# Optimization experiments

Measured on AMD Instinct MI355X. Metric: run time of the kernel, lower is better.

## Reference

```python
import jax, jax.numpy as jnp
import numpy as np

H = 128; D = 16; L = 4
NP_ = 50000; NL_ = 10000; EPP = 500000; ELP = 100000; EPL = 100000


def _rbf(d):
    # GaussianSmearing(start=0, stop=8, num_gaussians=16)
    off = jnp.linspace(0.0, 8.0, D)
    coeff = -0.5 / ((8.0 / (D - 1)) ** 2)
    x = d[:, None] - off[None, :]
    return jnp.exp(coeff * x * x)


def _layer_norm(x, w, b, eps=1e-5):
    mu = jnp.mean(x, axis=-1, keepdims=True)
    var = jnp.var(x, axis=-1, keepdims=True)
    return (x - mu) * jax.lax.rsqrt(var + eps) * w + b


def _block(x_src, x_dst, src, dst, ea, Wf_, bf_, Ws_, bs_, bnw, bnb, lnw, lnb):
    # CGConv message: z = [x_i(dst), x_j(src), edge_attr]
    z = jnp.concatenate([x_dst[dst], x_src[src], ea], axis=-1)  # [E, 2H+D]
    m = jax.nn.sigmoid(z @ Wf_ + bf_) * jax.nn.softplus(z @ Ws_ + bs_)
    agg = jax.ops.segment_sum(m, dst, num_segments=x_dst.shape[0])
    # BatchNorm1d in eval mode with running_mean=0, running_var=1
    agg = agg * (bnw / jnp.sqrt(1.0 + 1e-5)) + bnb
    out = agg + x_dst            # CGConv internal residual
    out = _layer_norm(out, lnw, lnb)
    out = jax.nn.relu(out)
    return out + x_dst           # ResidualCGConvBlock residual (dropout=identity in eval)


def setup_inputs() -> dict:
    key = jax.random.key(0)
    ks = jax.random.split(key, 16)
    s = lambda n: 1.0 / np.sqrt(n)
    inp = {
        'x_protein': jax.random.normal(ks[0], (NP_, 6), jnp.float32),
        'x_ligand': jax.random.normal(ks[1], (NL_, 6), jnp.float32),
        'ei_pp': jnp.stack([jax.random.randint(ks[2], (EPP,), 0, NP_),
                            jax.random.randint(ks[3], (EPP,), 0, NP_)]).astype(jnp.int32),
        'ea_pp': jax.random.uniform(ks[4], (EPP,), jnp.float32, 0.0, 8.0),
        'ei_lp': jnp.stack([jax.random.randint(ks[5], (ELP,), 0, NL_),
                            jax.random.randint(ks[6], (ELP,), 0, NP_)]).astype(jnp.int32),
        'ea_lp': jax.random.uniform(ks[7], (ELP,), jnp.float32, 0.0, 8.0),
        'ei_pl': jnp.stack([jax.random.randint(ks[8], (EPL,), 0, NP_),
                            jax.random.randint(ks[9], (EPL,), 0, NL_)]).astype(jnp.int32),
        'ea_pl': jax.random.uniform(ks[10], (EPL,), jnp.float32, 0.0, 8.0),
        'Wp': jax.random.normal(ks[11], (6, H), jnp.float32) * s(6),
        'bp': jnp.zeros((H,), jnp.float32),
        'Wl': jax.random.normal(ks[12], (6, H), jnp.float32) * s(6),
        'bl': jnp.zeros((H,), jnp.float32),
        'Wf': jax.random.normal(ks[13], (L, 3, 2 * H + D, H), jnp.float32) * s(2 * H + D),
        'bf': jnp.zeros((L, 3, H), jnp.float32),
        'Ws': jax.random.normal(ks[14], (L, 3, 2 * H + D, H), jnp.float32) * s(2 * H + D),
        'bs': jnp.zeros((L, 3, H), jnp.float32),
        'bn_w': jnp.ones((L, 3, H), jnp.float32),
        'bn_b': jnp.zeros((L, 3, H), jnp.float32),
        'ln_w': jnp.ones((L, 3, H), jnp.float32),
        'ln_b': jnp.zeros((L, 3, H), jnp.float32),
        'lno_w': jnp.ones((H,), jnp.float32),
        'lno_b': jnp.zeros((H,), jnp.float32),
        'fc_w': jax.random.normal(ks[15], (H, 21), jnp.float32) * s(H),
        'fc_b': jnp.zeros((21,), jnp.float32),
    }
    return inp


def reference(x_protein, x_ligand, ei_pp, ea_pp, ei_lp, ea_lp, ei_pl, ea_pl,
              Wp, bp, Wl, bl, Wf, bf, Ws, bs, bn_w, bn_b, ln_w, ln_b,
              lno_w, lno_b, fc_w, fc_b):
    xp = x_protein @ Wp + bp
    xl = x_ligand @ Wl + bl
    rpp = _rbf(ea_pp); rlp = _rbf(ea_lp); rpl = _rbf(ea_pl)
    for l in range(L):
        # HeteroConv aggr='sum': protein receives from pp and lp; ligand from pl
        p_pp = _block(xp, xp, ei_pp[0], ei_pp[1], rpp, Wf[l, 0], bf[l, 0], Ws[l, 0], bs[l, 0],
                      bn_w[l, 0], bn_b[l, 0], ln_w[l, 0], ln_b[l, 0])
        p_lp = _block(xl, xp, ei_lp[0], ei_lp[1], rlp, Wf[l, 1], bf[l, 1], Ws[l, 1], bs[l, 1],
                      bn_w[l, 1], bn_b[l, 1], ln_w[l, 1], ln_b[l, 1])
        l_pl = _block(xp, xl, ei_pl[0], ei_pl[1], rpl, Wf[l, 2], bf[l, 2], Ws[l, 2], bs[l, 2],
                      bn_w[l, 2], bn_b[l, 2], ln_w[l, 2], ln_b[l, 2])
        xp, xl = p_pp + p_lp, l_pl
    out = _layer_norm(xp, lno_w, lno_b)
    return out @ fc_w + fc_b
```

## Files before the change

### kernel.cpp

```cpp
#include <hip/hip_runtime.h>
#include <hip/hip_bf16.h>
#include <math.h>

#define H 128
#define LOG2E 1.44269504f

typedef _Float16 f16;
typedef _Float16 f16x2 __attribute__((ext_vector_type(2)));
typedef _Float16 f16x8 __attribute__((ext_vector_type(8)));
typedef float f32x4 __attribute__((ext_vector_type(4)));
typedef float f32x2 __attribute__((ext_vector_type(2)));
typedef unsigned int uint32;

union u2h { uint32 u; f16x2 h; };
static __device__ __forceinline__ f16x2 as_h2(uint32 v){ u2h x; x.u = v; return x.h; }
static __device__ __forceinline__ uint32 pack_h2(float a, float b){
  u2h p; p.h = (f16x2){(f16)a, (f16)b}; return p.u;
}

static __device__ __forceinline__ int unperm64(int r){
  int base = r & ~63; int g = r & 63; int t = g >> 4; int j = g & 15;
  return base + 4*j + t;
}

#define NBIN 256
#define PREP_WP_N (4*1024*128)
#define PREP_WL_N (4*512*128)
#define RBF_N     (12*(NBIN+1)*128)
#define FC_N      (32*128)

__global__ void prep_all(const float* __restrict__ Wf, const float* __restrict__ Ws,
                         const float* __restrict__ bfv, const float* __restrict__ bsv,
                         f16* __restrict__ Wt_p, float* __restrict__ Bias_p,
                         f16* __restrict__ Wt_l, float* __restrict__ Bias_l,
                         f16* __restrict__ T2,
                         const float* __restrict__ fcw,
                         f16* __restrict__ fwhi, f16* __restrict__ fwlo,
                         const float* __restrict__ Xp, const float* __restrict__ Wp,
                         const float* __restrict__ bp, f16* __restrict__ Xph, int NP,
                         const float* __restrict__ Xl, const float* __restrict__ Wl,
                         const float* __restrict__ bl, f16* __restrict__ Xlh, int NL){
  int t = blockIdx.x*blockDim.x + threadIdx.x;
  if (t < PREP_WP_N){
    int k = t & 127; int idx = t >> 7;
    int rs = idx & 1023; int l = idx >> 10;
    int r = unperm64(rs);
    int rel, c, row0; const float* W; float bias = 0.f;
    if (r < 512){
      rel = (r < 256) ? 0 : 2;
      int rr = r & 255; int j = rr & 3;
      W = (j >= 2) ? Ws : Wf;
      c = ((rr >> 2) << 1) | (j & 1);
      row0 = 128;
    }
    else if (r < 640) { rel=0; c=r-512; row0=0; W=Wf; bias = bfv[(l*3+rel)*H+c]; }
    else if (r < 768) { rel=0; c=r-640; row0=0; W=Ws; bias = bsv[(l*3+rel)*H+c]; }
    else if (r < 896) { rel=1; c=r-768; row0=0; W=Wf; bias = bfv[(l*3+rel)*H+c]; }
    else              { rel=1; c=r-896; row0=0; W=Ws; bias = bsv[(l*3+rel)*H+c]; }
    Wt_p[t] = (f16)(LOG2E * W[((size_t)(l*3+rel)*272 + row0 + k)*H + c]);
    if (k == 0) Bias_p[l*1024 + r] = LOG2E * bias;
    return;
  }
  t -= PREP_WP_N;
  if (t < PREP_WL_N){
    int k = t & 127; int idx = t >> 7;
    int rs = idx & 511; int l = idx >> 9;
    int r = unperm64(rs);
    int rel, c, row0; const float* W; float bias = 0.f;
    if (r < 256){
      rel = 1; int j = r & 3;
      W = (j >= 2) ? Ws : Wf;
      c = ((r >> 2) << 1) | (j & 1);
      row0 = 128;
    }
    else if (r < 384) { rel=2; c=r-256; row0=0; W=Wf; bias = bfv[(l*3+rel)*H+c]; }
    else              { rel=2; c=r-384; row0=0; W=Ws; bias = bsv[(l*3+rel)*H+c]; }
    Wt_l[t] = (f16)(LOG2E * W[((size_t)(l*3+rel)*272 + row0 + k)*H + c]);
    if (k == 0) Bias_l[l*512 + r] = LOG2E * bias;
    return;
  }
  t -= PREP_WL_N;
  if (t < RBF_N){
    int c = t & 127;
    int b = (t >> 7) % (NBIN+1);
    int pr = t / ((NBIN+1)*128);
    float d0 = (float)b * (8.0f/(float)NBIN);
    const float* wf = Wf + ((size_t)pr*272 + 256)*H + c;
    const float* ws = Ws + ((size_t)pr*272 + 256)*H + c;
    float f0=0.f, s0=0.f;
    #pragma unroll
    for (int k=0;k<16;k++){
      float o = 0.533333333f*(float)k;
      float tt = d0 - o;
      float r0 = __expf(-1.7578125f*tt*tt);
      f0 += r0*wf[(size_t)k*H]; s0 += r0*ws[(size_t)k*H];
    }
    f16* o = T2 + ((size_t)(pr*(NBIN+1) + b))*256;
    int m = c >> 1, sub = c & 1;
    o[4*m + sub]     = (f16)(LOG2E * f0);
    o[4*m + 2 + sub] = (f16)(LOG2E * s0);
    return;
  }
  t -= RBF_N;
  if (t < FC_N){
    int col = t >> 7, k = t & 127;
    float w = (col < 21) ? fcw[k*21 + col] : 0.f;
    f16 hi = (f16)w;
    fwhi[col*128 + k] = hi;
    fwlo[col*128 + k] = (f16)(w - (float)hi);
    return;
  }
  t -= FC_N;
  {
    int idx = t;
    const float* Xin; const float* W; const float* b; f16* Xh;
    if (idx < NP*H){ Xin=Xp; W=Wp; b=bp; Xh=Xph; }
    else { idx -= NP*H; if (idx >= NL*H) return; Xin=Xl; W=Wl; b=bl; Xh=Xlh; }
    int n = idx >> 7, c = idx & 127;
    float acc = b[c];
    #pragma unroll
    for (int k=0;k<6;k++) acc += Xin[n*6+k] * W[k*H+c];
    Xh[idx] = (f16)acc;
  }
}

__global__ void hist3_k(const int* __restrict__ dpp, int Epp,
                        const int* __restrict__ dlp, int Elp,
                        const int* __restrict__ dpl, int Epl,
                        int* __restrict__ cpp, int* __restrict__ clp, int* __restrict__ cpl){
  int e = blockIdx.x*blockDim.x + threadIdx.x;
  if (e < Epp) atomicAdd(&cpp[dpp[e]], 1);
  else if (e < Epp+Elp) atomicAdd(&clp[dlp[e-Epp]], 1);
  else if (e < Epp+Elp+Epl) atomicAdd(&cpl[dpl[e-Epp-Elp]], 1);
}

#define SCH 1024

__global__ void __launch_bounds__(256) chunksum_k(
    const int* __restrict__ counts, int NP, int NL, int Cpp, int Cpl,
    int* __restrict__ chsum){
  __shared__ int wred[4];
  int b = blockIdx.x;
  const int* cnt; int n; int ch;
  if (b < Cpp){ cnt = counts; n = NP; ch = b; }
  else if (b < 2*Cpp){ cnt = counts + NP; n = NP; ch = b - Cpp; }
  else { cnt = counts + 2*NP; n = NL; ch = b - 2*Cpp; }
  int base = ch * SCH;
  int tid = threadIdx.x;
  int s = 0;
  #pragma unroll
  for (int j=0;j<SCH/256;j++){
    int i = base + tid + j*256;
    if (i < n) s += cnt[i];
  }
  #pragma unroll
  for (int o=32;o>=1;o>>=1) s += __shfl_xor(s,o,64);
  if ((tid & 63) == 0) wred[tid>>6] = s;
  __syncthreads();
  if (tid == 0) chsum[b] = wred[0]+wred[1]+wred[2]+wred[3];
}

__global__ void __launch_bounds__(192) scanmid_k(
    int* __restrict__ chsum, int Cpp, int Cpl, int NP, int NL,
    int* __restrict__ rp_pp, int* __restrict__ rp_lp, int* __restrict__ rp_pl){
  int wid = threadIdx.x >> 6, lane = threadIdx.x & 63;
  int C, off; int* rp_end; int n;
  if (wid == 0){ C = Cpp; off = 0;      rp_end = rp_pp; n = NP; }
  else if (wid == 1){ C = Cpp; off = Cpp; rp_end = rp_lp; n = NP; }
  else { C = Cpl; off = 2*Cpp; rp_end = rp_pl; n = NL; }
  int v = (lane < C) ? chsum[off + lane] : 0;
  int x = v;
  #pragma unroll
  for (int o=1;o<64;o<<=1){
    int y = __shfl_up(x, o, 64);
    if (lane >= o) x += y;
  }
  if (lane < C) chsum[off + lane] = x - v;
  if (lane == 63) rp_end[n] = x;
}

__global__ void __launch_bounds__(1024) scanfin_k(
    const int* __restrict__ counts, int NP, int NL, int Cpp, int Cpl,
    const int* __restrict__ chsum,
    int* __restrict__ rp_pp, int* __restrict__ cur_pp,
    int* __restrict__ rp_lp, int* __restrict__ cur_lp,
    int* __restrict__ rp_pl, int* __restrict__ cur_pl){
  __shared__ int wsum[16];
  int b = blockIdx.x;
  const int* cnt; int n, ch; int* rp; int* cur;
  if (b < Cpp){ cnt = counts; n = NP; ch = b; rp = rp_pp; cur = cur_pp; }
  else if (b < 2*Cpp){ cnt = counts + NP; n = NP; ch = b - Cpp; rp = rp_lp; cur = cur_lp; }
  else { cnt = counts + 2*NP; n = NL; ch = b - 2*Cpp; rp = rp_pl; cur = cur_pl; }
  int tid = threadIdx.x, lane = tid & 63, wid = tid >> 6;
  int i = ch*SCH + tid;
  int v = (i < n) ? cnt[i] : 0;
  int x = v;
  #pragma unroll
  for (int o=1;o<64;o<<=1){
    int y = __shfl_up(x, o, 64);
    if (lane >= o) x += y;
  }
  if (lane == 63) wsum[wid] = x;
  __syncthreads();
  if (wid == 0 && lane < 16){
    int w = wsum[lane];
    #pragma unroll
    for (int o=1;o<16;o<<=1){
      int y = __shfl_up(w, o, 64);
      if (lane >= o) w += y;
    }
    wsum[lane] = w;
  }
  __syncthreads();
  int waveoff = (wid == 0) ? 0 : wsum[wid-1];
  int ex = chsum[b] + waveoff + x - v;
  if (i < n){ rp[i] = ex; cur[i] = ex; }
}

__global__ void fill3_k(const int* __restrict__ ei_pp, const float* __restrict__ ea_pp, int Epp,
                        const int* __restrict__ ei_lp, const float* __restrict__ ea_lp, int Elp,
                        const int* __restrict__ ei_pl, const float* __restrict__ ea_pl, int Epl,
                        int* __restrict__ cur_pp, int2* __restrict__ e2_pp,
                        int* __restrict__ cur_lp, int2* __restrict__ e2_lp,
                        int* __restrict__ cur_pl, int2* __restrict__ e2_pl){
  int e = blockIdx.x*blockDim.x + threadIdx.x;
  if (e < Epp){
    int p = atomicAdd(&cur_pp[ei_pp[Epp + e]], 1);
    e2_pp[p] = make_int2(ei_pp[e], __float_as_int(ea_pp[e]));
  } else if (e < Epp+Elp){
    int i = e - Epp;
    int p = atomicAdd(&cur_lp[ei_lp[Elp + i]], 1);
    e2_lp[p] = make_int2(ei_lp[i], __float_as_int(ea_lp[i]));
  } else if (e < Epp+Elp+Epl){
    int i = e - Epp - Elp;
    int p = atomicAdd(&cur_pl[ei_pl[Epl + i]], 1);
    e2_pl[p] = make_int2(ei_pl[i], __float_as_int(ea_pl[i]));
  }
}

__global__ void __launch_bounds__(256) degbin_hist(
    const int* __restrict__ rp_pp, const int* __restrict__ rp_lp,
    const int* __restrict__ rp_pl, int NP, int NL, int* __restrict__ hist){
  __shared__ int lh[128];
  int t = threadIdx.x;
  if (t < 128) lh[t] = 0;
  __syncthreads();
  int i = blockIdx.x*256 + t;
  if (i < NP){
    int d = (rp_pp[i+1]-rp_pp[i]) + (rp_lp[i+1]-rp_lp[i]);
    if (d > 63) d = 63;
    atomicAdd(&lh[63 - d], 1);
  } else if (i < NP+NL){
    int n = i - NP;
    int d = rp_pl[n+1]-rp_pl[n];
    if (d > 63) d = 63;
    atomicAdd(&lh[64 + 63 - d], 1);
  }
  __syncthreads();
  if (t < 128 && lh[t]) atomicAdd(&hist[t], lh[t]);
}

__global__ void __launch_bounds__(128) degbin_scan(
    const int* __restrict__ hist, int* __restrict__ cursor){
  int t = threadIdx.x, lane = t & 63;
  int v = hist[t];
  int x = v;
  #pragma unroll
  for (int o=1;o<64;o<<=1){
    int y = __shfl_up(x, o, 64);
    if (lane >= o) x += y;
  }
  cursor[t] = x - v;
}

__global__ void __launch_bounds__(256) degbin_scatter(
    const int* __restrict__ rp_pp, const int* __restrict__ rp_lp,
    const int* __restrict__ rp_pl, int NP, int NL,
    int* __restrict__ cursor, int* __restrict__ perm){
  __shared__ int lh[128], lbase[128], lrank[128];
  int t = threadIdx.x;
  if (t < 128){ lh[t] = 0; lrank[t] = 0; }
  __syncthreads();
  int i = blockIdx.x*256 + t;
  int bin = -1, n = 0;
  if (i < NP){
    n = i;
    int d = (rp_pp[i+1]-rp_pp[i]) + (rp_lp[i+1]-rp_lp[i]);
    if (d > 63) d = 63;
    bin = 63 - d;
  } else if (i < NP+NL){
    n = i - NP;
    int d = rp_pl[n+1]-rp_pl[n];
    if (d > 63) d = 63;
    bin = 64 + 63 - d;
  }
  if (bin >= 0) atomicAdd(&lh[bin], 1);
  __syncthreads();
  if (t < 128 && lh[t]) lbase[t] = atomicAdd(&cursor[t], lh[t]);
  __syncthreads();
  if (bin >= 0){
    int r = atomicAdd(&lrank[bin], 1);
    perm[(bin < 64 ? 0 : NP) + lbase[bin] + r] = n;
  }
}

#define GR 8
__global__ void __launch_bounds__(256) gemm_tables(
    const f16* __restrict__ Xp, const f16* __restrict__ Wtp,
    const float* __restrict__ Biasp, f16* __restrict__ Outp,
    int strips_p, int tasks_p,
    const f16* __restrict__ Xl, const f16* __restrict__ Wtl,
    const float* __restrict__ Biasl, f16* __restrict__ Outl,
    int strips_l, int tasks_total){
  int wt = blockIdx.x*4 + (threadIdx.x >> 6);
  if (wt >= tasks_total) return;
  const f16 *X, *Wt; const float* Bias; f16* Out; int N, strips, g, chunk;
  if (wt < tasks_p){
    X=Xp; Wt=Wtp; Bias=Biasp; Out=Outp; N=1024; strips=strips_p;
    g = wt & 15; chunk = wt >> 4;
  } else {
    int w = wt - tasks_p;
    X=Xl; Wt=Wtl; Bias=Biasl; Out=Outl; N=512; strips=strips_l;
    g = w & 7; chunk = w >> 3;
  }
  int n0 = g << 6;
  int lane = threadIdx.x & 63;
  int lr = lane & 15, lq = lane >> 4;
  const f16x8* B0 = (const f16x8*)(const void*)(Wt + (size_t)(n0      + lr)*H);
  const f16x8* B1 = (const f16x8*)(const void*)(Wt + (size_t)(n0 + 16 + lr)*H);
  const f16x8* B2 = (const f16x8*)(const void*)(Wt + (size_t)(n0 + 32 + lr)*H);
  const f16x8* B3 = (const f16x8*)(const void*)(Wt + (size_t)(n0 + 48 + lr)*H);
  f16x8 b0_0=B0[lq], b0_1=B0[4+lq], b0_2=B0[8+lq], b0_3=B0[12+lq];
  f16x8 b1_0=B1[lq], b1_1=B1[4+lq], b1_2=B1[8+lq], b1_3=B1[12+lq];
  f16x8 b2_0=B2[lq], b2_1=B2[4+lq], b2_2=B2[8+lq], b2_3=B2[12+lq];
  f16x8 b3_0=B3[lq], b3_1=B3[4+lq], b3_2=B3[8+lq], b3_3=B3[12+lq];
  float4 bias = ((const float4*)(const void*)(Bias + n0))[lr];
  #pragma unroll 2
  for (int r=0;r<GR;r++){
    int strip = chunk*GR + r;
    if (strip >= strips) break;
    int m0 = strip << 4;
    const f16x8* A = (const f16x8*)(const void*)(X + (size_t)(m0+lr)*H);
    f16x8 a0 = A[lq], a1 = A[4+lq], a2 = A[8+lq], a3 = A[12+lq];
    f32x4 acc0 = {0.f,0.f,0.f,0.f}, acc1 = acc0, acc2 = acc0, acc3 = acc0;
    acc0 = __builtin_amdgcn_mfma_f32_16x16x32_f16(a0, b0_0, acc0, 0, 0, 0);
    acc1 = __builtin_amdgcn_mfma_f32_16x16x32_f16(a0, b1_0, acc1, 0, 0, 0);
    acc2 = __builtin_amdgcn_mfma_f32_16x16x32_f16(a0, b2_0, acc2, 0, 0, 0);
    acc3 = __builtin_amdgcn_mfma_f32_16x16x32_f16(a0, b3_0, acc3, 0, 0, 0);
    acc0 = __builtin_amdgcn_mfma_f32_16x16x32_f16(a1, b0_1, acc0, 0, 0, 0);
    acc1 = __builtin_amdgcn_mfma_f32_16x16x32_f16(a1, b1_1, acc1, 0, 0, 0);
    acc2 = __builtin_amdgcn_mfma_f32_16x16x32_f16(a1, b2_1, acc2, 0, 0, 0);
    acc3 = __builtin_amdgcn_mfma_f32_16x16x32_f16(a1, b3_1, acc3, 0, 0, 0);
    acc0 = __builtin_amdgcn_mfma_f32_16x16x32_f16(a2, b0_2, acc0, 0, 0, 0);
    acc1 = __builtin_amdgcn_mfma_f32_16x16x32_f16(a2, b1_2, acc1, 0, 0, 0);
    acc2 = __builtin_amdgcn_mfma_f32_16x16x32_f16(a2, b2_2, acc2, 0, 0, 0);
    acc3 = __builtin_amdgcn_mfma_f32_16x16x32_f16(a2, b3_2, acc3, 0, 0, 0);
    acc0 = __builtin_amdgcn_mfma_f32_16x16x32_f16(a3, b0_3, acc0, 0, 0, 0);
    acc1 = __builtin_amdgcn_mfma_f32_16x16x32_f16(a3, b1_3, acc1, 0, 0, 0);
    acc2 = __builtin_amdgcn_mfma_f32_16x16x32_f16(a3, b2_3, acc2, 0, 0, 0);
    acc3 = __builtin_amdgcn_mfma_f32_16x16x32_f16(a3, b3_3, acc3, 0, 0, 0);
    #pragma unroll
    for (int rr=0;rr<4;rr++){
      int row = m0 + lq*4 + rr;
      uint2 pk;
      pk.x = pack_h2(acc0[rr] + bias.x, acc1[rr] + bias.y);
      pk.y = pack_h2(acc2[rr] + bias.z, acc3[rr] + bias.w);
      *(uint2*)(void*)(Out + (size_t)row*N + n0 + 4*lr) = pk;
    }
  }
}

static __device__ __forceinline__ float act_msg(float F, float S){
  float sig = __builtin_amdgcn_rcpf(1.f + __builtin_amdgcn_exp2f(-F));
  float e   = __builtin_amdgcn_exp2f(fminf(S, 86.f));
  float sp  = 0.69314718f * __builtin_amdgcn_logf(1.f + e);
  return sig * sp;
}

#define BN_RSQ 0.9999950000374997f

static __device__ __forceinline__ void edge_nb(uint2 g, uint2 t,
                                               f16x2 fd2, f16x2 sd2, f32x2& acc){
  f16x2 F = (as_h2(g.x) + as_h2(t.x)) + fd2;
  f16x2 S = (as_h2(g.y) + as_h2(t.y)) + sd2;
  acc.x += act_msg((float)F.x, (float)S.x);
  acc.y += act_msg((float)F.y, (float)S.y);
}

static __device__ __forceinline__ void ln_stats_w(float v0, float v1, float& mu, float& var){
  float s = v0 + v1, q = v0*v0 + v1*v1;
  #pragma unroll
  for (int o=32;o>=1;o>>=1){ s += __shfl_xor(s,o,64); q += __shfl_xor(q,o,64); }
  mu = s * (1.f/128.f);
  var = q * (1.f/128.f) - mu*mu;
}

static __device__ __forceinline__ void aggregate(
    const int2* __restrict__ ev_arr, int e0, int e1,
    const uint2* __restrict__ G, int gstride, int goff,
    const uint2* __restrict__ Tb, int lane,
    f16x2 fd2, f16x2 sd2, f32x2& acc)
{
  for (int base = e0; base < e1; base += 64){
    int idx = base + lane;
    int2 ev = ev_arr[(idx < e1) ? idx : (e1-1)];
    float dd = __int_as_float(ev.y);
    int bnv = (int)__fmaf_rn(dd, (float)NBIN/8.0f, 0.5f);
    bnv = (bnv > NBIN) ? NBIN : bnv;
    int cnt = e1 - base; cnt = (cnt > 64) ? 64 : cnt;
    uint2 gA, tA, gB, tB, gC, tC;
    #define LDJ(gX, tX, j) { \
      int s_ = __builtin_amdgcn_readlane(ev.x, (j)); \
      int b_ = __builtin_amdgcn_readlane(bnv, (j)); \
      gX = G[(size_t)s_*gstride + goff + lane]; \
      tX = Tb[(size_t)b_*64 + lane]; }
    LDJ(gA, tA, 0);
    if (cnt > 1) LDJ(gB, tB, 1);
    if (cnt > 2) LDJ(gC, tC, 2);
    int j = 0;
    for (; j+5 < cnt; j += 3){
      edge_nb(gA, tA, fd2, sd2, acc); LDJ(gA, tA, j+3);
      edge_nb(gB, tB, fd2, sd2, acc); LDJ(gB, tB, j+4);
      edge_nb(gC, tC, fd2, sd2, acc); LDJ(gC, tC, j+5);
    }
    int rem = cnt - j;
    edge_nb(gA, tA, fd2, sd2, acc);
    if (rem > 3) LDJ(gA, tA, j+3);
    if (rem > 1) edge_nb(gB, tB, fd2, sd2, acc);
    if (rem > 4) LDJ(gB, tB, j+4);
    if (rem > 2) edge_nb(gC, tC, fd2, sd2, acc);
    if (rem > 3) edge_nb(gA, tA, fd2, sd2, acc);
    if (rem > 4) edge_nb(gB, tB, fd2, sd2, acc);
    #undef LDJ
  }
}

__global__ void __launch_bounds__(256) node_update(
    const f16* __restrict__ PT, const f16* __restrict__ LT,
    const f16* __restrict__ xp, const f16* __restrict__ xl,
    const int* __restrict__ pp_rp, const int2* __restrict__ pp_e2,
    const int* __restrict__ lp_rp, const int2* __restrict__ lp_e2,
    const int* __restrict__ pl_rp, const int2* __restrict__ pl_e2,
    const f16* __restrict__ T2,
    const float* __restrict__ bn_w, const float* __restrict__ bn_b,
    const float* __restrict__ ln_w, const float* __restrict__ ln_b,
    const int* __restrict__ perm,
    f16* __restrict__ xp_o, f16* __restrict__ xl_o,
    int layer, int NP, int NL, int PB)
{
  int wave = threadIdx.x >> 6;
  int lane = threadIdx.x & 63;
  const uint2* PTg = (const uint2*)(const void*)PT;
  if ((int)blockIdx.x < PB){
    int idx = blockIdx.x*4 + wave;
    if (idx >= NP) return;
    int node = perm[idx];
    f16x2 xh = as_h2(((const uint32*)(const void*)xp)[(size_t)node*64 + lane]);
    float xx = (float)xh.x, xy = (float)xh.y;
    const uint32* PTu = (const uint32*)(const void*)PT;
    const uint2*  LTg = (const uint2*)(const void*)LT;
    float o1_0, o1_1, o2_0, o2_1;
    {
      int pr = layer*3 + 0;
      f16x2 fd2 = as_h2(PTu[(size_t)node*512 + 256 + lane]);
      f16x2 sd2 = as_h2(PTu[(size_t)node*512 + 320 + lane]);
      const uint2* Tb = (const uint2*)(const void*)(T2 + (size_t)pr*(NBIN+1)*256);
      f32x2 acc = {0.f, 0.f};
      aggregate(pp_e2, pp_rp[node], pp_rp[node+1], PTg, 256, 0, Tb, lane, fd2, sd2, acc);
      float2 bw = ((const float2*)(const void*)(bn_w + pr*H))[lane];
      float2 bb = ((const float2*)(const void*)(bn_b + pr*H))[lane];
      float2 lw = ((const float2*)(const void*)(ln_w + pr*H))[lane];
      float2 lb = ((const float2*)(const void*)(ln_b + pr*H))[lane];
      float v0 = acc.x * (bw.x * BN_RSQ) + bb.x + xx;
      float v1 = acc.y * (bw.y * BN_RSQ) + bb.y + xy;
      float mu, var; ln_stats_w(v0, v1, mu, var);
      float rs = rsqrtf(var + 1e-5f);
      o1_0 = fmaxf((v0-mu)*rs*lw.x + lb.x, 0.f) + xx;
      o1_1 = fmaxf((v1-mu)*rs*lw.y + lb.y, 0.f) + xy;
    }
    {
      int pr = layer*3 + 1;
      f16x2 fd2 = as_h2(PTu[(size_t)node*512 + 384 + lane]);
      f16x2 sd2 = as_h2(PTu[(size_t)node*512 + 448 + lane]);
      const uint2* Tb = (const uint2*)(const void*)(T2 + (size_t)pr*(NBIN+1)*256);
      f32x2 acc = {0.f, 0.f};
      aggregate(lp_e2, lp_rp[node], lp_rp[node+1], LTg, 128, 0, Tb, lane, fd2, sd2, acc);
      float2 bw = ((const float2*)(const void*)(bn_w + pr*H))[lane];
      float2 bb = ((const float2*)(const void*)(bn_b + pr*H))[lane];
      float2 lw = ((const float2*)(const void*)(ln_w + pr*H))[lane];
      float2 lb = ((const float2*)(const void*)(ln_b + pr*H))[lane];
      float v0 = acc.x * (bw.x * BN_RSQ) + bb.x + xx;
      float v1 = acc.y * (bw.y * BN_RSQ) + bb.y + xy;
      float mu, var; ln_stats_w(v0, v1, mu, var);
      float rs = rsqrtf(var + 1e-5f);
      o2_0 = fmaxf((v0-mu)*rs*lw.x + lb.x, 0.f) + xx;
      o2_1 = fmaxf((v1-mu)*rs*lw.y + lb.y, 0.f) + xy;
    }
    float out0 = o1_0 + o2_0, out1 = o1_1 + o2_1;
    ((uint32*)(void*)xp_o)[(size_t)node*64 + lane] = pack_h2(out0, out1);
  } else {
    int idx = (blockIdx.x - PB)*4 + wave;
    if (idx >= NL) return;
    int node = perm[NP + idx];
    f16x2 xh = as_h2(((const uint32*)(const void*)xl)[(size_t)node*64 + lane]);
    float xx = (float)xh.x, xy = (float)xh.y;
    const uint32* LTu = (const uint32*)(const void*)LT;
    int pr = layer*3 + 2;
    f16x2 fd2 = as_h2(LTu[(size_t)node*256 + 128 + lane]);
    f16x2 sd2 = as_h2(LTu[(size_t)node*256 + 192 + lane]);
    const uint2* Tb = (const uint2*)(const void*)(T2 + (size_t)pr*(NBIN+1)*256);
    f32x2 acc = {0.f, 0.f};
    aggregate(pl_e2, pl_rp[node], pl_rp[node+1], PTg, 256, 64, Tb, lane, fd2, sd2, acc);
    float2 bw = ((const float2*)(const void*)(bn_w + pr*H))[lane];
    float2 bb = ((const float2*)(const void*)(bn_b + pr*H))[lane];
    float2 lw = ((const float2*)(const void*)(ln_w + pr*H))[lane];
    float2 lb = ((const float2*)(const void*)(ln_b + pr*H))[lane];
    float v0 = acc.x * (bw.x * BN_RSQ) + bb.x + xx;
    float v1 = acc.y * (bw.y * BN_RSQ) + bb.y + xy;
    float mu, var; ln_stats_w(v0, v1, mu, var);
    float rs = rsqrtf(var + 1e-5f);
    float out0 = fmaxf((v0-mu)*rs*lw.x + lb.x, 0.f) + xx;
    float out1 = fmaxf((v1-mu)*rs*lw.y + lb.y, 0.f) + xy;
    ((uint32*)(void*)xl_o)[(size_t)node*64 + lane] = pack_h2(out0, out1);
  }
}

__global__ void __launch_bounds__(256) final_k(const f16* __restrict__ xp,
    const float* __restrict__ lnw, const float* __restrict__ lnb,
    const f16* __restrict__ fwhi, const f16* __restrict__ fwlo,
    const float* __restrict__ fcb, float* __restrict__ out, int N){
  int wave = threadIdx.x >> 6, lane = threadIdx.x & 63;
  int m0 = (blockIdx.x*4 + wave) << 4;
  if (m0 >= N) return;
  int lr = lane & 15, lq = lane >> 4;
  int node = m0 + lr; if (node >= N) node = N - 1;
  const f16x8* X = (const f16x8*)(const void*)(xp + (size_t)node*H);
  f16x8 x0 = X[lq], x1 = X[4+lq], x2 = X[8+lq], x3 = X[12+lq];
  float s = 0.f, q = 0.f;
  #pragma unroll
  for (int i=0;i<8;i++){
    float a=(float)x0[i], b=(float)x1[i], c=(float)x2[i], d=(float)x3[i];
    s += a+b+c+d; q += a*a+b*b+c*c+d*d;
  }
  s += __shfl_xor(s,16,64); q += __shfl_xor(q,16,64);
  s += __shfl_xor(s,32,64); q += __shfl_xor(q,32,64);
  float mu = s*(1.f/128.f), var = q*(1.f/128.f) - mu*mu;
  float rs = rsqrtf(var + 1e-5f);
  f16x8 xs0 = x0, xs1 = x1, xs2 = x2, xs3 = x3;
  f16x8 ah[4], al[4];
  const float4* LW = (const float4*)(const void*)lnw;
  const float4* LB = (const float4*)(const void*)lnb;
  #define MKFRAG(F, XS) { \
    int b4 = F*8 + lq*2; \
    float4 w0 = LW[b4], w1 = LW[b4+1]; \
    float4 c0 = LB[b4], c1 = LB[b4+1]; \
    float l0=((float)XS[0]-mu)*rs*w0.x + c0.x; \
    float l1=((float)XS[1]-mu)*rs*w0.y + c0.y; \
    float l2=((float)XS[2]-mu)*rs*w0.z + c0.z; \
    float l3=((float)XS[3]-mu)*rs*w0.w + c0.w; \
    float l4=((float)XS[4]-mu)*rs*w1.x + c1.x; \
    float l5=((float)XS[5]-mu)*rs*w1.y + c1.y; \
    float l6=((float)XS[6]-mu)*rs*w1.z + c1.z; \
    float l7=((float)XS[7]-mu)*rs*w1.w + c1.w; \
    f16x8 hh = {(f16)l0,(f16)l1,(f16)l2,(f16)l3,(f16)l4,(f16)l5,(f16)l6,(f16)l7}; \
    f16x8 ll = {(f16)(l0-(float)hh[0]),(f16)(l1-(float)hh[1]), \
                (f16)(l2-(float)hh[2]),(f16)(l3-(float)hh[3]), \
                (f16)(l4-(float)hh[4]),(f16)(l5-(float)hh[5]), \
                (f16)(l6-(float)hh[6]),(f16)(l7-(float)hh[7])}; \
    ah[F] = hh; al[F] = ll; }
  MKFRAG(0, xs0); MKFRAG(1, xs1); MKFRAG(2, xs2); MKFRAG(3, xs3);
  #undef MKFRAG
  const f16x8* BH0 = (const f16x8*)(const void*)(fwhi + (size_t)lr*128);
  const f16x8* BH1 = (const f16x8*)(const void*)(fwhi + (size_t)(16+lr)*128);
  const f16x8* BL0 = (const f16x8*)(const void*)(fwlo + (size_t)lr*128);
  const f16x8* BL1 = (const f16x8*)(const void*)(fwlo + (size_t)(16+lr)*128);
  f32x4 acc0 = {0.f,0.f,0.f,0.f}, acc1 = acc0;
  #pragma unroll
  for (int f=0; f<4; f++){
    f16x8 bh0 = BH0[f*4+lq], bh1 = BH1[f*4+lq];
    f16x8 bl0 = BL0[f*4+lq], bl1 = BL1[f*4+lq];
    acc0 = __builtin_amdgcn_mfma_f32_16x16x32_f16(ah[f], bh0, acc0, 0, 0, 0);
    acc1 = __builtin_amdgcn_mfma_f32_16x16x32_f16(ah[f], bh1, acc1, 0, 0, 0);
    acc0 = __builtin_amdgcn_mfma_f32_16x16x32_f16(al[f], bh0, acc0, 0, 0, 0);
    acc1 = __builtin_amdgcn_mfma_f32_16x16x32_f16(al[f], bh1, acc1, 0, 0, 0);
    acc0 = __builtin_amdgcn_mfma_f32_16x16x32_f16(ah[f], bl0, acc0, 0, 0, 0);
    acc1 = __builtin_amdgcn_mfma_f32_16x16x32_f16(ah[f], bl1, acc1, 0, 0, 0);
  }
  float bias0 = fcb[lr];
  float bias1 = (lr < 5) ? fcb[16 + lr] : 0.f;
  #pragma unroll
  for (int rr=0; rr<4; rr++){
    int row = m0 + lq*4 + rr;
    if (row < N){
      out[(size_t)row*21 + lr] = acc0[rr] + bias0;
      if (lr < 5) out[(size_t)row*21 + 16 + lr] = acc1[rr] + bias1;
    }
  }
}

extern "C" void kernel_launch(void* const* d_in, const int* in_sizes, int n_in,
                              void* d_out, int out_size, void* d_ws, size_t ws_size,
                              hipStream_t stream){
  const float* x_protein = (const float*)d_in[0];
  const float* x_ligand  = (const float*)d_in[1];
  const int*   ei_pp = (const int*)d_in[2];
  const float* ea_pp = (const float*)d_in[3];
  const int*   ei_lp = (const int*)d_in[4];
  const float* ea_lp = (const float*)d_in[5];
  const int*   ei_pl = (const int*)d_in[6];
  const float* ea_pl = (const float*)d_in[7];
  const float* Wp  = (const float*)d_in[8];
  const float* bp  = (const float*)d_in[9];
  const float* Wl  = (const float*)d_in[10];
  const float* bl  = (const float*)d_in[11];
  const float* Wf  = (const float*)d_in[12];
  const float* bfv = (const float*)d_in[13];
  const float* Wsv = (const float*)d_in[14];
  const float* bsv = (const float*)d_in[15];
  const float* bn_w = (const float*)d_in[16];
  const float* bn_b = (const float*)d_in[17];
  const float* ln_w = (const float*)d_in[18];
  const float* ln_b = (const float*)d_in[19];
  const float* lno_w = (const float*)d_in[20];
  const float* lno_b = (const float*)d_in[21];
  const float* fc_w = (const float*)d_in[22];
  const float* fc_b = (const float*)d_in[23];

  int NP  = in_sizes[0]/6, NL = in_sizes[1]/6;
  int EPP = in_sizes[3], ELP = in_sizes[5], EPL = in_sizes[7];

  char* ws = (char*)d_ws;
  size_t off = 0;
  auto alloc = [&](size_t bytes)->void*{
    void* p = ws + off; off = (off + bytes + 255) & ~(size_t)255; return p;
  };

  f16* xpA = (f16*)alloc((size_t)NP*H*2);
  f16* xpB = (f16*)alloc((size_t)NP*H*2);
  f16* xlA = (f16*)alloc((size_t)NL*H*2);
  f16* xlB = (f16*)alloc((size_t)NL*H*2);
  f16* PT    = (f16*)alloc((size_t)NP*1024*2);
  f16* LT    = (f16*)alloc((size_t)NL*512*2);
  f16* Wt_p  = (f16*)alloc((size_t)4*1024*H*2);
  f16* Wt_l  = (f16*)alloc((size_t)4*512*H*2);
  float* Bias_p = (float*)alloc((size_t)4*1024*4);
  float* Bias_l = (float*)alloc((size_t)4*512*4);
  f16* T2    = (f16*)alloc((size_t)12*(NBIN+1)*256*2);
  f16* fwhi  = (f16*)alloc((size_t)32*128*2);
  f16* fwlo  = (f16*)alloc((size_t)32*128*2);
  int* counts = (int*)alloc((size_t)(2*NP+NL)*4);
  int* rp_pp  = (int*)alloc((size_t)(NP+1)*4);
  int* cur_pp = (int*)alloc((size_t)NP*4);
  int* rp_lp  = (int*)alloc((size_t)(NP+1)*4);
  int* cur_lp = (int*)alloc((size_t)NP*4);
  int* rp_pl  = (int*)alloc((size_t)(NL+1)*4);
  int* cur_pl = (int*)alloc((size_t)NL*4);
  int2* e2_pp = (int2*)alloc((size_t)EPP*8);
  int2* e2_lp = (int2*)alloc((size_t)ELP*8);
  int2* e2_pl = (int2*)alloc((size_t)EPL*8);
  int Cpp = (NP + SCH - 1) / SCH;
  int Cpl = (NL + SCH - 1) / SCH;
  int* chsum = (int*)alloc((size_t)(2*Cpp + Cpl)*4);
  int* dhist  = (int*)alloc(128*4);
  int* dcur   = (int*)alloc(128*4);
  int* perm   = (int*)alloc((size_t)(NP+NL)*4);
  (void)ws_size; (void)n_in; (void)out_size;

  size_t prep_total = (size_t)PREP_WP_N + PREP_WL_N + RBF_N + FC_N + (size_t)(NP+NL)*H;
  prep_all<<<(prep_total+255)/256, 256, 0, stream>>>(Wf, Wsv, bfv, bsv,
      Wt_p, Bias_p, Wt_l, Bias_l, T2,
      fc_w, fwhi, fwlo,
      x_protein, Wp, bp, xpA, NP,
      x_ligand,  Wl, bl, xlA, NL);
  hipMemsetAsync(counts, 0, (size_t)(2*NP+NL)*4, stream);
  hipMemsetAsync(dhist, 0, 128*4, stream);
  int* cnt_pp = counts; int* cnt_lp = counts + NP; int* cnt_pl = counts + 2*NP;
  int Etot = EPP + ELP + EPL;
  hist3_k<<<(Etot+255)/256, 256, 0, stream>>>(ei_pp+EPP, EPP, ei_lp+ELP, ELP, ei_pl+EPL, EPL,
                                              cnt_pp, cnt_lp, cnt_pl);
  chunksum_k<<<2*Cpp + Cpl, 256, 0, stream>>>(counts, NP, NL, Cpp, Cpl, chsum);
  scanmid_k<<<1, 192, 0, stream>>>(chsum, Cpp, Cpl, NP, NL, rp_pp, rp_lp, rp_pl);
  scanfin_k<<<2*Cpp + Cpl, 1024, 0, stream>>>(counts, NP, NL, Cpp, Cpl, chsum,
                                              rp_pp, cur_pp, rp_lp, cur_lp, rp_pl, cur_pl);
  fill3_k<<<(Etot+255)/256, 256, 0, stream>>>(ei_pp, ea_pp, EPP, ei_lp, ea_lp, ELP,
                                              ei_pl, ea_pl, EPL,
                                              cur_pp, e2_pp, cur_lp, e2_lp, cur_pl, e2_pl);
  int nbks = (NP + NL + 255) / 256;
  degbin_hist<<<nbks, 256, 0, stream>>>(rp_pp, rp_lp, rp_pl, NP, NL, dhist);
  degbin_scan<<<1, 128, 0, stream>>>(dhist, dcur);
  degbin_scatter<<<nbks, 256, 0, stream>>>(rp_pp, rp_lp, rp_pl, NP, NL, dcur, perm);

  f16* xp_cur = xpA; f16* xp_nxt = xpB;
  f16* xl_cur = xlA; f16* xl_nxt = xlB;
  int strips_p = NP >> 4, strips_l = NL >> 4;
  int tasks_p = 16 * ((strips_p + GR - 1) / GR);
  int tasks_l = 8  * ((strips_l + GR - 1) / GR);
  int tasks_total = tasks_p + tasks_l;
  int PB = (NP + 3) / 4, LB = (NL + 3) / 4;
  for (int l=0; l<4; l++){
    gemm_tables<<<(tasks_total+3)/4, 256, 0, stream>>>(
        xp_cur, Wt_p + (size_t)l*1024*H, Bias_p + l*1024, PT, strips_p, tasks_p,
        xl_cur, Wt_l + (size_t)l*512*H,  Bias_l + l*512,  LT, strips_l, tasks_total);
    node_update<<<PB + LB, 256, 0, stream>>>(PT, LT, xp_cur, xl_cur,
        rp_pp, e2_pp, rp_lp, e2_lp, rp_pl, e2_pl, T2,
        bn_w, bn_b, ln_w, ln_b, perm, xp_nxt, xl_nxt, l, NP, NL, PB);
    f16* t;
    t = xp_cur; xp_cur = xp_nxt; xp_nxt = t;
    t = xl_cur; xl_cur = xl_nxt; xl_nxt = t;
  }

  int fstrips = (NP + 15) >> 4;
  final_k<<<(fstrips+3)/4, 256, 0, stream>>>(xp_cur, lno_w, lno_b,
      fwhi, fwlo, fc_b, (float*)d_out, NP);
}
```

Before: 685.2 us.

## Remap GEMM block tasks, fold ln2 into BN scale, shrink node_update blocks

The gemm_tables task mapping is reordered so each block's four waves share one row chunk and work on adjacent column groups, with chunks grouped in eights. This is meant to improve L2 reuse of the X rows and weight tiles. The softplus ln2 multiply is removed from the per-edge activation and folded into the BatchNorm scale constant, saving one multiply per edge element. node_update now launches 128-thread blocks (two waves per block) instead of 256, giving finer-grained scheduling of the degree-sorted nodes and less tail imbalance at the cost of more blocks.

```diff
diff --git a/kernel.cpp b/kernel.cpp
--- a/kernel.cpp
+++ b/kernel.cpp
@@ -308,20 +308,24 @@
 __global__ void __launch_bounds__(256) gemm_tables(
     const f16* __restrict__ Xp, const f16* __restrict__ Wtp,
     const float* __restrict__ Biasp, f16* __restrict__ Outp,
-    int strips_p, int tasks_p,
+    int strips_p, int chunks_p, int pblocks,
     const f16* __restrict__ Xl, const f16* __restrict__ Wtl,
     const float* __restrict__ Biasl, f16* __restrict__ Outl,
-    int strips_l, int tasks_total){
-  int wt = blockIdx.x*4 + (threadIdx.x >> 6);
-  if (wt >= tasks_total) return;
+    int strips_l, int chunks_l){
+  int b = blockIdx.x;
+  int w = threadIdx.x >> 6;
   const f16 *X, *Wt; const float* Bias; f16* Out; int N, strips, g, chunk;
-  if (wt < tasks_p){
+  if (b < pblocks){
+    int c = (b >> 5)*8 + (b & 7);
+    if (c >= chunks_p) return;
     X=Xp; Wt=Wtp; Bias=Biasp; Out=Outp; N=1024; strips=strips_p;
-    g = wt & 15; chunk = wt >> 4;
+    g = ((b >> 3) & 3)*4 + w; chunk = c;
   } else {
-    int w = wt - tasks_p;
+    int bl = b - pblocks;
+    int c = (bl >> 4)*8 + (bl & 7);
+    if (c >= chunks_l) return;
     X=Xl; Wt=Wtl; Bias=Biasl; Out=Outl; N=512; strips=strips_l;
-    g = w & 7; chunk = w >> 3;
+    g = ((bl >> 3) & 1)*4 + w; chunk = c;
   }
   int n0 = g << 6;
   int lane = threadIdx.x & 63;
@@ -373,11 +377,10 @@
 static __device__ __forceinline__ float act_msg(float F, float S){
   float sig = __builtin_amdgcn_rcpf(1.f + __builtin_amdgcn_exp2f(-F));
   float e   = __builtin_amdgcn_exp2f(fminf(S, 86.f));
-  float sp  = 0.69314718f * __builtin_amdgcn_logf(1.f + e);
-  return sig * sp;
-}
-
-#define BN_RSQ 0.9999950000374997f
+  return sig * __builtin_amdgcn_logf(1.f + e);
+}
+
+#define BN_SCL (0.9999950000374997f * 0.69314718f)
 
 static __device__ __forceinline__ void edge_nb(uint2 g, uint2 t,
                                                f16x2 fd2, f16x2 sd2, f32x2& acc){
@@ -435,7 +438,7 @@
   }
 }
 
-__global__ void __launch_bounds__(256) node_update(
+__global__ void __launch_bounds__(128) node_update(
     const f16* __restrict__ PT, const f16* __restrict__ LT,
     const f16* __restrict__ xp, const f16* __restrict__ xl,
     const int* __restrict__ pp_rp, const int2* __restrict__ pp_e2,
@@ -452,7 +455,7 @@
   int lane = threadIdx.x & 63;
   const uint2* PTg = (const uint2*)(const void*)PT;
   if ((int)blockIdx.x < PB){
-    int idx = blockIdx.x*4 + wave;
+    int idx = blockIdx.x*2 + wave;
     if (idx >= NP) return;
     int node = perm[idx];
     f16x2 xh = as_h2(((const uint32*)(const void*)xp)[(size_t)node*64 + lane]);
@@ -471,8 +474,8 @@
       float2 bb = ((const float2*)(const void*)(bn_b + pr*H))[lane];
       float2 lw = ((const float2*)(const void*)(ln_w + pr*H))[lane];
       float2 lb = ((const float2*)(const void*)(ln_b + pr*H))[lane];
-      float v0 = acc.x * (bw.x * BN_RSQ) + bb.x + xx;
-      float v1 = acc.y * (bw.y * BN_RSQ) + bb.y + xy;
+      float v0 = acc.x * (bw.x * BN_SCL) + bb.x + xx;
+      float v1 = acc.y * (bw.y * BN_SCL) + bb.y + xy;
       float mu, var; ln_stats_w(v0, v1, mu, var);
       float rs = rsqrtf(var + 1e-5f);
       o1_0 = fmaxf((v0-mu)*rs*lw.x + lb.x, 0.f) + xx;
@@ -489,8 +492,8 @@
       float2 bb = ((const float2*)(const void*)(bn_b + pr*H))[lane];
       float2 lw = ((const float2*)(const void*)(ln_w + pr*H))[lane];
       float2 lb = ((const float2*)(const void*)(ln_b + pr*H))[lane];
-      float v0 = acc.x * (bw.x * BN_RSQ) + bb.x + xx;
-      float v1 = acc.y * (bw.y * BN_RSQ) + bb.y + xy;
+      float v0 = acc.x * (bw.x * BN_SCL) + bb.x + xx;
+      float v1 = acc.y * (bw.y * BN_SCL) + bb.y + xy;
       float mu, var; ln_stats_w(v0, v1, mu, var);
       float rs = rsqrtf(var + 1e-5f);
       o2_0 = fmaxf((v0-mu)*rs*lw.x + lb.x, 0.f) + xx;
@@ -499,7 +502,7 @@
     float out0 = o1_0 + o2_0, out1 = o1_1 + o2_1;
     ((uint32*)(void*)xp_o)[(size_t)node*64 + lane] = pack_h2(out0, out1);
   } else {
-    int idx = (blockIdx.x - PB)*4 + wave;
+    int idx = (blockIdx.x - PB)*2 + wave;
     if (idx >= NL) return;
     int node = perm[NP + idx];
     f16x2 xh = as_h2(((const uint32*)(const void*)xl)[(size_t)node*64 + lane]);
@@ -515,8 +518,8 @@
     float2 bb = ((const float2*)(const void*)(bn_b + pr*H))[lane];
     float2 lw = ((const float2*)(const void*)(ln_w + pr*H))[lane];
     float2 lb = ((const float2*)(const void*)(ln_b + pr*H))[lane];
-    float v0 = acc.x * (bw.x * BN_RSQ) + bb.x + xx;
-    float v1 = acc.y * (bw.y * BN_RSQ) + bb.y + xy;
+    float v0 = acc.x * (bw.x * BN_SCL) + bb.x + xx;
+    float v1 = acc.y * (bw.y * BN_SCL) + bb.y + xy;
     float mu, var; ln_stats_w(v0, v1, mu, var);
     float rs = rsqrtf(var + 1e-5f);
     float out0 = fmaxf((v0-mu)*rs*lw.x + lb.x, 0.f) + xx;
@@ -693,15 +696,16 @@
   f16* xp_cur = xpA; f16* xp_nxt = xpB;
   f16* xl_cur = xlA; f16* xl_nxt = xlB;
   int strips_p = NP >> 4, strips_l = NL >> 4;
-  int tasks_p = 16 * ((strips_p + GR - 1) / GR);
-  int tasks_l = 8  * ((strips_l + GR - 1) / GR);
-  int tasks_total = tasks_p + tasks_l;
-  int PB = (NP + 3) / 4, LB = (NL + 3) / 4;
+  int chunks_p = (strips_p + GR - 1) / GR;
+  int chunks_l = (strips_l + GR - 1) / GR;
+  int pblocks = ((chunks_p + 7) / 8) * 32;
+  int lblocks = ((chunks_l + 7) / 8) * 16;
+  int PB = (NP + 1) / 2, LB = (NL + 1) / 2;
   for (int l=0; l<4; l++){
-    gemm_tables<<<(tasks_total+3)/4, 256, 0, stream>>>(
-        xp_cur, Wt_p + (size_t)l*1024*H, Bias_p + l*1024, PT, strips_p, tasks_p,
-        xl_cur, Wt_l + (size_t)l*512*H,  Bias_l + l*512,  LT, strips_l, tasks_total);
-    node_update<<<PB + LB, 256, 0, stream>>>(PT, LT, xp_cur, xl_cur,
+    gemm_tables<<<pblocks + lblocks, 256, 0, stream>>>(
+        xp_cur, Wt_p + (size_t)l*1024*H, Bias_p + l*1024, PT, strips_p, chunks_p, pblocks,
+        xl_cur, Wt_l + (size_t)l*512*H,  Bias_l + l*512,  LT, strips_l, chunks_l);
+    node_update<<<PB + LB, 128, 0, stream>>>(PT, LT, xp_cur, xl_cur,
         rp_pp, e2_pp, rp_lp, e2_lp, rp_pl, e2_pl, T2,
         bn_w, bn_b, ln_w, ln_b, perm, xp_nxt, xl_nxt, l, NP, NL, PB);
     f16* t;
```

Result: no change. 680.8 us (median of 2 runs) (-0.6%).
